# Kernel tuning notes

Measured on AMD Instinct MI355X. Metric: run time of the kernel, lower is better.

## Reference

```python
import jax, jax.numpy as jnp
import numpy as np

TAU, RHO, OFFSET, DELTA, START = 0.01, 100.0, 1.44, 0.05, 0.5
N_LEVELS = 3


def _heaviside(x):
    # torch.heaviside(x, values=1.0): 0 for x<0, 1 for x==0, 1 for x>0
    return jnp.where(x < 0, 0.0, 1.0).astype(x.dtype)


def _tau_sigmoid(x, tau):
    # 1 / (1 + exp(clamp(-x/tau, -50, 50)))
    e = jnp.clip(-x / tau, -50.0, 50.0)
    return 1.0 / (1.0 + jnp.exp(e))


def _step_rank(x, target):
    # x: [B, B, B] score diffs; target: [B, B] int relevance counts
    # inferior_relevance[b, i, j] = target[b, i] > target[b, j]
    inferior = target[:, :, None] > target[:, None, :]
    pos = x > 0
    margin = x > DELTA
    sig = _tau_sigmoid(x, TAU)
    pos_branch = jnp.where(margin, RHO * (x - DELTA) + OFFSET, START + sig)
    inf_val = jnp.where(pos, pos_branch, sig)
    return jnp.where(inferior, inf_val, _heaviside(x))


def setup_inputs() -> dict:
    key = jax.random.key(0)
    k1, k2 = jax.random.split(key)
    B, D = 384, 512
    emb = jax.random.normal(k1, (B, D), dtype=jnp.float32)
    emb = emb / jnp.linalg.norm(emb, axis=-1, keepdims=True)  # cosine-sim embeddings
    labels = jax.random.randint(k2, (B, N_LEVELS), 0, 8, dtype=jnp.int64)
    return {"embeddings": emb, "labels": labels}


def reference(embeddings, labels):
    B = embeddings.shape[0]
    scores = embeddings @ embeddings.T                      # [B, B]
    # create_label_matrix: count of matching hierarchy levels
    target = (labels[:, None, :] == labels[None, :, :]).sum(-1)  # [B, B] int
    relevances = target.astype(scores.dtype) / N_LEVELS          # [B, B]

    mask = 1.0 - jnp.eye(B, dtype=scores.dtype)             # [B, B] (broadcast over batch)
    # sim_diff[b, i, j] = scores[b, j] - scores[b, i]
    sim_diff = scores[:, None, :] - scores[:, :, None]      # [B, B, B]
    min_rel = jnp.minimum(relevances[:, :, None], relevances[:, None, :])

    rank = 1.0 + jnp.sum(_step_rank(sim_diff, target) * mask, axis=-1)      # [B, B]
    hrank = relevances + jnp.sum(_heaviside(sim_diff) * min_rel * mask, axis=-1)

    mhap = (hrank / rank).sum(-1) / relevances.sum(-1)      # [B]
    return jnp.mean(1.0 - mhap)                             # return_type='1-mHAP', reduce='mean'
```

## Files before the change

kernel.cpp:

```cpp
#include <hip/hip_runtime.h>
#include <hip/hip_bf16.h>

#define NB 384
#define ND 512

__global__ __launch_bounds__(256) void gemm_scores(const float* __restrict__ emb,
                                                   float* __restrict__ s0,
                                                   float* __restrict__ s1) {
    __shared__ float As[32][65];
    __shared__ float Bs[32][65];
    const int tid = threadIdx.x;
    const int tx = tid & 15, ty = tid >> 4;
    const int i0 = blockIdx.y * 32, j0 = blockIdx.x * 32;
    const int kbase = blockIdx.z * (ND / 2);
    float* __restrict__ s = blockIdx.z ? s1 : s0;
    float acc00 = 0.f, acc01 = 0.f, acc10 = 0.f, acc11 = 0.f;

    for (int k0 = kbase; k0 < kbase + ND / 2; k0 += 64) {
#pragma unroll
        for (int p = 0; p < 2; ++p) {
            int idx = tid + 256 * p;
            int r = idx >> 4;
            int c = (idx & 15) << 2;
            float4 av = *reinterpret_cast<const float4*>(emb + (i0 + r) * ND + k0 + c);
            As[r][c] = av.x; As[r][c + 1] = av.y; As[r][c + 2] = av.z; As[r][c + 3] = av.w;
            float4 bv = *reinterpret_cast<const float4*>(emb + (j0 + r) * ND + k0 + c);
            Bs[r][c] = bv.x; Bs[r][c + 1] = bv.y; Bs[r][c + 2] = bv.z; Bs[r][c + 3] = bv.w;
        }
        __syncthreads();
#pragma unroll 8
        for (int kk = 0; kk < 64; ++kk) {
            float a0 = As[2 * ty][kk], a1 = As[2 * ty + 1][kk];
            float b0 = Bs[2 * tx][kk], b1 = Bs[2 * tx + 1][kk];
            acc00 = fmaf(a0, b0, acc00); acc01 = fmaf(a0, b1, acc01);
            acc10 = fmaf(a1, b0, acc10); acc11 = fmaf(a1, b1, acc11);
        }
        __syncthreads();
    }
    const int i = i0 + 2 * ty, j = j0 + 2 * tx;
    s[i * NB + j]           = acc00; s[i * NB + j + 1]       = acc01;
    s[(i + 1) * NB + j]     = acc10; s[(i + 1) * NB + j + 1] = acc11;
}

__global__ __launch_bounds__(NB) void hap_prep(const float* __restrict__ s0,
                                               const float* __restrict__ s1,
                                               const int* __restrict__ labels,
                                               float* __restrict__ g,
                                               int* __restrict__ offs,
                                               float* __restrict__ tsumArr) {
    __shared__ int wcnt[6][4];
    __shared__ int wbase[6][4];
    __shared__ int cbase[4];
    const int tid = threadIdx.x, lane = tid & 63, wv = tid >> 6;
    const int b = blockIdx.x;
    const int l0 = labels[b * 3 + 0], l1 = labels[b * 3 + 1], l2 = labels[b * 3 + 2];
    const int t = (labels[tid * 3 + 0] == l0) + (labels[tid * 3 + 1] == l1) +
                  (labels[tid * 3 + 2] == l2);
    const float sv = s0[b * NB + tid] + s1[b * NB + tid];
    const unsigned long long mlt = (1ull << lane) - 1ull;
    int myrank = 0;
#pragma unroll
    for (int c = 0; c < 4; ++c) {
        unsigned long long m = __ballot(t == c);
        if (t == c) myrank = __popcll(m & mlt);
        if (lane == 0) wcnt[wv][c] = __popcll(m);
    }
    __syncthreads();
    if (tid == 0) {
        int tot0 = 0, tot1 = 0, tot2 = 0, tot3 = 0;
        for (int w = 0; w < 6; ++w) {
            wbase[w][0] = tot0; tot0 += wcnt[w][0];
            wbase[w][1] = tot1; tot1 += wcnt[w][1];
            wbase[w][2] = tot2; tot2 += wcnt[w][2];
            wbase[w][3] = tot3; tot3 += wcnt[w][3];
        }
        cbase[0] = 0; cbase[1] = tot0; cbase[2] = tot0 + tot1; cbase[3] = tot0 + tot1 + tot2;
        offs[b * 4 + 0] = cbase[1];
        offs[b * 4 + 1] = cbase[2];
        offs[b * 4 + 2] = cbase[3];
        tsumArr[b] = (float)(tot1 + 2 * tot2 + 3 * tot3);
    }
    __syncthreads();
    g[b * NB + cbase[t] + wbase[wv][t] + myrank] = sv;
}

__global__ __launch_bounds__(192) void hap_part(const float* __restrict__ g,
                                                const int* __restrict__ offs,
                                                float2* __restrict__ part) {
    __shared__ alignas(16) float gs[96];
    const int tid = threadIdx.x;
    const int b = blockIdx.x, ih = blockIdx.y, jh = blockIdx.z;
    const int q0 = jh * 96;

    if (tid < 96) gs[tid] = g[b * NB + q0 + tid];
    const int i = ih * 192 + tid;
    const float si = g[b * NB + i];
    const int S1 = offs[b * 4 + 0], S2 = offs[b * 4 + 1], S3 = offs[b * 4 + 2];
    const int ti = (i >= S1) + (i >= S2) + (i >= S3);
    __syncthreads();

    const int Rti = (ti == 0) ? 0 : (ti == 1) ? S1 : (ti == 2) ? S2 : S3;
    int m = Rti - q0; m = m < 0 ? 0 : (m > 96 ? 96 : m);

    const float nsiK = si * 144.26950408889634f;
    const float pconst = fmaf(-100.f, si, -3.56f);
    const float c1 = si + 0.05f;

    float rs = 0.f, hs = 0.f;
    int k = 0;
#pragma unroll 4
    for (; k < m; ++k) {
        const float sj = gs[k];
        const float ex = __builtin_amdgcn_exp2f(fmaf(sj, -144.26950408889634f, nsiK));
        const float sg = __builtin_amdgcn_rcpf(1.f + ex);
        const float posb = fmaf(100.f, sj, pconst);
        const float sel = (sj > c1) ? posb : (0.5f + sg);
        rs += (sj > si) ? sel : sg;
        const int pos = q0 + k;
        const float wk = (float)((pos >= S1) + (pos >= S2));
        hs += (sj >= si) ? wk : 0.f;
    }
    int cnt = 0;
#pragma unroll 8
    for (; k < 96; ++k) cnt += (gs[k] >= si) ? 1 : 0;

    rs += (float)cnt;
    hs += (float)(ti * cnt);
    part[(jh * NB + b) * NB + i] = make_float2(rs, hs);
}

__global__ __launch_bounds__(192) void hap_combine(const float2* __restrict__ part,
                                                   const float* __restrict__ tsumArr,
                                                   float* __restrict__ bsum) {
    __shared__ float redQ[3];
    const int tid = threadIdx.x, lane = tid & 63, wv = tid >> 6;
    const int b = blockIdx.x;
    float q = 0.f;
#pragma unroll
    for (int rep = 0; rep < 2; ++rep) {
        const int i = rep * 192 + tid;
        float r = 0.f, h = 0.f;
#pragma unroll
        for (int jh = 0; jh < 4; ++jh) {
            const float2 p = part[(jh * NB + b) * NB + i];
            r += p.x; h += p.y;
        }
        q += h / r;
    }
#pragma unroll
    for (int off = 32; off > 0; off >>= 1) q += __shfl_xor(q, off, 64);
    if (lane == 0) redQ[wv] = q;
    __syncthreads();
    if (tid == 0) bsum[b] = (redQ[0] + redQ[1] + redQ[2]) / (tsumArr[b] * (float)NB);
}

__global__ __launch_bounds__(64) void hap_final(const float* __restrict__ bsum,
                                                float* __restrict__ out) {
    const int tid = threadIdx.x;
    float p = 0.f;
    for (int k = tid; k < NB; k += 64) p += bsum[k];
#pragma unroll
    for (int off = 32; off > 0; off >>= 1) p += __shfl_xor(p, off, 64);
    if (tid == 0) out[0] = 1.f - p;
}

extern "C" void kernel_launch(void* const* d_in, const int* in_sizes, int n_in,
                              void* d_out, int out_size, void* d_ws, size_t ws_size,
                              hipStream_t stream) {
    const float* emb = (const float*)d_in[0];
    const int* labels = (const int*)d_in[1];
    float* out = (float*)d_out;

    float* s0 = (float*)d_ws;
    float* s1 = s0 + NB * NB;
    float* g  = s1 + NB * NB;
    float2* part = (float2*)(g + NB * NB);
    int* offs = (int*)(part + 4 * NB * NB);
    float* tsumArr = (float*)(offs + NB * 4);
    float* bsum = tsumArr + NB;

    gemm_scores<<<dim3(12, 12, 2), 256, 0, stream>>>(emb, s0, s1);
    hap_prep<<<NB, NB, 0, stream>>>(s0, s1, labels, g, offs, tsumArr);
    hap_part<<<dim3(NB, 2, 4), 192, 0, stream>>>(g, offs, part);
    hap_combine<<<NB, 192, 0, stream>>>(part, tsumArr, bsum);
    hap_final<<<1, 64, 0, stream>>>(bsum, out);
}
```

Before: 46.06 us.

## Fuse prep, partial and combine kernels; retile GEMM with 8-way split-K

Merges the bucket-sort prep, pairwise partial, and combine kernels into one kernel per (row, quarter). Each block redoes the label-grouped sort in shared memory and reduces its partials with shuffles instead of writing intermediate arrays. The GEMM moves to 64x64 tiles with 4x4 register blocking, a transposed LDS layout with float4 reads, and 8 split-K slices. This cuts launches and global round trips, but the sort and the 8-slice score summation are now repeated 4 times per row.

```diff
diff --git a/kernel.cpp b/kernel.cpp
--- a/kernel.cpp
+++ b/kernel.cpp
@@ -3,66 +3,83 @@
 
 #define NB 384
 #define ND 512
+#define NZ 8
 
 __global__ __launch_bounds__(256) void gemm_scores(const float* __restrict__ emb,
-                                                   float* __restrict__ s0,
-                                                   float* __restrict__ s1) {
-    __shared__ float As[32][65];
-    __shared__ float Bs[32][65];
+                                                   float* __restrict__ sp) {
+    __shared__ alignas(16) float At[64 * 68];
+    __shared__ alignas(16) float Bt[64 * 68];
     const int tid = threadIdx.x;
+    const int i0 = blockIdx.y * 64, j0 = blockIdx.x * 64;
+    const int kb = blockIdx.z * 64;
+    float* __restrict__ s = sp + blockIdx.z * (NB * NB);
+
+#pragma unroll
+    for (int p = 0; p < 4; ++p) {
+        const int idx = tid + 256 * p;
+        const int r = idx >> 4;
+        const int c4 = (idx & 15) << 2;
+        const float4 av = *reinterpret_cast<const float4*>(emb + (i0 + r) * ND + kb + c4);
+        At[(c4 + 0) * 68 + r] = av.x;
+        At[(c4 + 1) * 68 + r] = av.y;
+        At[(c4 + 2) * 68 + r] = av.z;
+        At[(c4 + 3) * 68 + r] = av.w;
+        const float4 bv = *reinterpret_cast<const float4*>(emb + (j0 + r) * ND + kb + c4);
+        Bt[(c4 + 0) * 68 + r] = bv.x;
+        Bt[(c4 + 1) * 68 + r] = bv.y;
+        Bt[(c4 + 2) * 68 + r] = bv.z;
+        Bt[(c4 + 3) * 68 + r] = bv.w;
+    }
+    __syncthreads();
+
     const int tx = tid & 15, ty = tid >> 4;
-    const int i0 = blockIdx.y * 32, j0 = blockIdx.x * 32;
-    const int kbase = blockIdx.z * (ND / 2);
-    float* __restrict__ s = blockIdx.z ? s1 : s0;
-    float acc00 = 0.f, acc01 = 0.f, acc10 = 0.f, acc11 = 0.f;
-
-    for (int k0 = kbase; k0 < kbase + ND / 2; k0 += 64) {
+    float acc[4][4] = {};
+#pragma unroll 4
+    for (int kk = 0; kk < 64; ++kk) {
+        const float4 a = *reinterpret_cast<const float4*>(&At[kk * 68 + ty * 4]);
+        const float4 b = *reinterpret_cast<const float4*>(&Bt[kk * 68 + tx * 4]);
+        acc[0][0] = fmaf(a.x, b.x, acc[0][0]); acc[0][1] = fmaf(a.x, b.y, acc[0][1]);
+        acc[0][2] = fmaf(a.x, b.z, acc[0][2]); acc[0][3] = fmaf(a.x, b.w, acc[0][3]);
+        acc[1][0] = fmaf(a.y, b.x, acc[1][0]); acc[1][1] = fmaf(a.y, b.y, acc[1][1]);
+        acc[1][2] = fmaf(a.y, b.z, acc[1][2]); acc[1][3] = fmaf(a.y, b.w, acc[1][3]);
+        acc[2][0] = fmaf(a.z, b.x, acc[2][0]); acc[2][1] = fmaf(a.z, b.y, acc[2][1]);
+        acc[2][2] = fmaf(a.z, b.z, acc[2][2]); acc[2][3] = fmaf(a.z, b.w, acc[2][3]);
+        acc[3][0] = fmaf(a.w, b.x, acc[3][0]); acc[3][1] = fmaf(a.w, b.y, acc[3][1]);
+        acc[3][2] = fmaf(a.w, b.z, acc[3][2]); acc[3][3] = fmaf(a.w, b.w, acc[3][3]);
+    }
 #pragma unroll
-        for (int p = 0; p < 2; ++p) {
-            int idx = tid + 256 * p;
-            int r = idx >> 4;
-            int c = (idx & 15) << 2;
-            float4 av = *reinterpret_cast<const float4*>(emb + (i0 + r) * ND + k0 + c);
-            As[r][c] = av.x; As[r][c + 1] = av.y; As[r][c + 2] = av.z; As[r][c + 3] = av.w;
-            float4 bv = *reinterpret_cast<const float4*>(emb + (j0 + r) * ND + k0 + c);
-            Bs[r][c] = bv.x; Bs[r][c + 1] = bv.y; Bs[r][c + 2] = bv.z; Bs[r][c + 3] = bv.w;
-        }
-        __syncthreads();
-#pragma unroll 8
-        for (int kk = 0; kk < 64; ++kk) {
-            float a0 = As[2 * ty][kk], a1 = As[2 * ty + 1][kk];
-            float b0 = Bs[2 * tx][kk], b1 = Bs[2 * tx + 1][kk];
-            acc00 = fmaf(a0, b0, acc00); acc01 = fmaf(a0, b1, acc01);
-            acc10 = fmaf(a1, b0, acc10); acc11 = fmaf(a1, b1, acc11);
-        }
-        __syncthreads();
+    for (int u = 0; u < 4; ++u) {
+        float4 o = make_float4(acc[u][0], acc[u][1], acc[u][2], acc[u][3]);
+        *reinterpret_cast<float4*>(&s[(i0 + ty * 4 + u) * NB + j0 + tx * 4]) = o;
     }
-    const int i = i0 + 2 * ty, j = j0 + 2 * tx;
-    s[i * NB + j]           = acc00; s[i * NB + j + 1]       = acc01;
-    s[(i + 1) * NB + j]     = acc10; s[(i + 1) * NB + j + 1] = acc11;
 }
 
-__global__ __launch_bounds__(NB) void hap_prep(const float* __restrict__ s0,
-                                               const float* __restrict__ s1,
-                                               const int* __restrict__ labels,
-                                               float* __restrict__ g,
-                                               int* __restrict__ offs,
-                                               float* __restrict__ tsumArr) {
+__global__ __launch_bounds__(384) void hap_fused(const float* __restrict__ sp,
+                                                 const int* __restrict__ labels,
+                                                 float* __restrict__ bpart) {
+    __shared__ alignas(16) float gs[NB];
     __shared__ int wcnt[6][4];
     __shared__ int wbase[6][4];
-    __shared__ int cbase[4];
+    __shared__ int cb[4];
+    __shared__ float tsum_sh;
+    __shared__ float redQ[6];
+
     const int tid = threadIdx.x, lane = tid & 63, wv = tid >> 6;
-    const int b = blockIdx.x;
+    const int b = blockIdx.x, iq = blockIdx.y;
+
     const int l0 = labels[b * 3 + 0], l1 = labels[b * 3 + 1], l2 = labels[b * 3 + 2];
     const int t = (labels[tid * 3 + 0] == l0) + (labels[tid * 3 + 1] == l1) +
                   (labels[tid * 3 + 2] == l2);
-    const float sv = s0[b * NB + tid] + s1[b * NB + tid];
+    float sv = 0.f;
+#pragma unroll
+    for (int z = 0; z < NZ; ++z) sv += sp[z * NB * NB + b * NB + tid];
+
     const unsigned long long mlt = (1ull << lane) - 1ull;
-    int myrank = 0;
+    int rk = 0;
 #pragma unroll
     for (int c = 0; c < 4; ++c) {
         unsigned long long m = __ballot(t == c);
-        if (t == c) myrank = __popcll(m & mlt);
+        if (t == c) rk = __popcll(m & mlt);
         if (lane == 0) wcnt[wv][c] = __popcll(m);
     }
     __syncthreads();
@@ -74,94 +91,72 @@
             wbase[w][2] = tot2; tot2 += wcnt[w][2];
             wbase[w][3] = tot3; tot3 += wcnt[w][3];
         }
-        cbase[0] = 0; cbase[1] = tot0; cbase[2] = tot0 + tot1; cbase[3] = tot0 + tot1 + tot2;
-        offs[b * 4 + 0] = cbase[1];
-        offs[b * 4 + 1] = cbase[2];
-        offs[b * 4 + 2] = cbase[3];
-        tsumArr[b] = (float)(tot1 + 2 * tot2 + 3 * tot3);
+        cb[0] = 0; cb[1] = tot0; cb[2] = tot0 + tot1; cb[3] = tot0 + tot1 + tot2;
+        tsum_sh = (float)(tot1 + 2 * tot2 + 3 * tot3);
     }
     __syncthreads();
-    g[b * NB + cbase[t] + wbase[wv][t] + myrank] = sv;
-}
-
-__global__ __launch_bounds__(192) void hap_part(const float* __restrict__ g,
-                                                const int* __restrict__ offs,
-                                                float2* __restrict__ part) {
-    __shared__ alignas(16) float gs[96];
-    const int tid = threadIdx.x;
-    const int b = blockIdx.x, ih = blockIdx.y, jh = blockIdx.z;
-    const int q0 = jh * 96;
-
-    if (tid < 96) gs[tid] = g[b * NB + q0 + tid];
-    const int i = ih * 192 + tid;
-    const float si = g[b * NB + i];
-    const int S1 = offs[b * 4 + 0], S2 = offs[b * 4 + 1], S3 = offs[b * 4 + 2];
-    const int ti = (i >= S1) + (i >= S2) + (i >= S3);
+    gs[cb[t] + wbase[wv][t] + rk] = sv;
     __syncthreads();
 
+    const int S1 = cb[1], S2 = cb[2], S3 = cb[3];
+    const int it = tid >> 2, jt = tid & 3;
+    const int i = iq * 96 + it;
+    const float si = gs[i];
+    const int ti = (i >= S1) + (i >= S2) + (i >= S3);
     const int Rti = (ti == 0) ? 0 : (ti == 1) ? S1 : (ti == 2) ? S2 : S3;
-    int m = Rti - q0; m = m < 0 ? 0 : (m > 96 ? 96 : m);
 
-    const float nsiK = si * 144.26950408889634f;
+    const float siK = si * 144.26950408889634f;
     const float pconst = fmaf(-100.f, si, -3.56f);
     const float c1 = si + 0.05f;
 
-    float rs = 0.f, hs = 0.f;
-    int k = 0;
-#pragma unroll 4
-    for (; k < m; ++k) {
+    float rs = 0.f;
+    int hsI = 0, cnt = 0;
+    for (int k = jt; k < Rti; k += 4) {
         const float sj = gs[k];
-        const float ex = __builtin_amdgcn_exp2f(fmaf(sj, -144.26950408889634f, nsiK));
+        const float ex = __builtin_amdgcn_exp2f(fmaf(sj, -144.26950408889634f, siK));
         const float sg = __builtin_amdgcn_rcpf(1.f + ex);
-        const float posb = fmaf(100.f, sj, pconst);
-        const float sel = (sj > c1) ? posb : (0.5f + sg);
+        const float ramp = fmaf(100.f, sj, pconst);
+        const float sel = (sj > c1) ? ramp : (0.5f + sg);
         rs += (sj > si) ? sel : sg;
-        const int pos = q0 + k;
-        const float wk = (float)((pos >= S1) + (pos >= S2));
-        hs += (sj >= si) ? wk : 0.f;
+        const int wk = (k >= S1) + (k >= S2);
+        hsI += (sj >= si) ? wk : 0;
     }
-    int cnt = 0;
-#pragma unroll 8
-    for (; k < 96; ++k) cnt += (gs[k] >= si) ? 1 : 0;
+    const int a0 = (Rti + 3) & ~3;
+    if (Rti + jt < a0) cnt += (gs[Rti + jt] >= si) ? 1 : 0;
+    const float4* gv = reinterpret_cast<const float4*>(gs);
+    for (int k4 = (a0 >> 2) + jt; k4 < (NB >> 2); k4 += 4) {
+        const float4 v = gv[k4];
+        cnt += ((v.x >= si) ? 1 : 0) + ((v.y >= si) ? 1 : 0) +
+               ((v.z >= si) ? 1 : 0) + ((v.w >= si) ? 1 : 0);
+    }
+    rs += (float)cnt;
+    hsI += ti * cnt;
 
-    rs += (float)cnt;
-    hs += (float)(ti * cnt);
-    part[(jh * NB + b) * NB + i] = make_float2(rs, hs);
-}
-
-__global__ __launch_bounds__(192) void hap_combine(const float2* __restrict__ part,
-                                                   const float* __restrict__ tsumArr,
-                                                   float* __restrict__ bsum) {
-    __shared__ float redQ[3];
-    const int tid = threadIdx.x, lane = tid & 63, wv = tid >> 6;
-    const int b = blockIdx.x;
-    float q = 0.f;
-#pragma unroll
-    for (int rep = 0; rep < 2; ++rep) {
-        const int i = rep * 192 + tid;
-        float r = 0.f, h = 0.f;
-#pragma unroll
-        for (int jh = 0; jh < 4; ++jh) {
-            const float2 p = part[(jh * NB + b) * NB + i];
-            r += p.x; h += p.y;
-        }
-        q += h / r;
-    }
+    rs += __shfl_xor(rs, 1); rs += __shfl_xor(rs, 2);
+    float hs = (float)hsI;
+    hs += __shfl_xor(hs, 1); hs += __shfl_xor(hs, 2);
+    float q = hs / rs;
 #pragma unroll
     for (int off = 32; off > 0; off >>= 1) q += __shfl_xor(q, off, 64);
     if (lane == 0) redQ[wv] = q;
     __syncthreads();
-    if (tid == 0) bsum[b] = (redQ[0] + redQ[1] + redQ[2]) / (tsumArr[b] * (float)NB);
+    if (tid == 0) {
+        const float tot = redQ[0] + redQ[1] + redQ[2] + redQ[3] + redQ[4] + redQ[5];
+        bpart[b * 4 + iq] = tot / (4.f * tsum_sh * (float)NB);
+    }
 }
 
-__global__ __launch_bounds__(64) void hap_final(const float* __restrict__ bsum,
-                                                float* __restrict__ out) {
-    const int tid = threadIdx.x;
+__global__ __launch_bounds__(256) void hap_final(const float* __restrict__ bpart,
+                                                 float* __restrict__ out) {
+    __shared__ float red[4];
+    const int tid = threadIdx.x, lane = tid & 63, wv = tid >> 6;
     float p = 0.f;
-    for (int k = tid; k < NB; k += 64) p += bsum[k];
+    for (int k = tid; k < NB * 4; k += 256) p += bpart[k];
 #pragma unroll
     for (int off = 32; off > 0; off >>= 1) p += __shfl_xor(p, off, 64);
-    if (tid == 0) out[0] = 1.f - p;
+    if (lane == 0) red[wv] = p;
+    __syncthreads();
+    if (tid == 0) out[0] = 1.f - (red[0] + red[1] + red[2] + red[3]);
 }
 
 extern "C" void kernel_launch(void* const* d_in, const int* in_sizes, int n_in,
@@ -171,17 +166,10 @@
     const int* labels = (const int*)d_in[1];
     float* out = (float*)d_out;
 
-    float* s0 = (float*)d_ws;
-    float* s1 = s0 + NB * NB;
-    float* g  = s1 + NB * NB;
-    float2* part = (float2*)(g + NB * NB);
-    int* offs = (int*)(part + 4 * NB * NB);
-    float* tsumArr = (float*)(offs + NB * 4);
-    float* bsum = tsumArr + NB;
+    float* sp = (float*)d_ws;
+    float* bpart = sp + NZ * NB * NB;
 
-    gemm_scores<<<dim3(12, 12, 2), 256, 0, stream>>>(emb, s0, s1);
-    hap_prep<<<NB, NB, 0, stream>>>(s0, s1, labels, g, offs, tsumArr);
-    hap_part<<<dim3(NB, 2, 4), 192, 0, stream>>>(g, offs, part);
-    hap_combine<<<NB, 192, 0, stream>>>(part, tsumArr, bsum);
-    hap_final<<<1, 64, 0, stream>>>(bsum, out);
+    gemm_scores<<<dim3(6, 6, NZ), 256, 0, stream>>>(emb, sp);
+    hap_fused<<<dim3(NB, 4), 384, 0, stream>>>(sp, labels, bpart);
+    hap_final<<<1, 256, 0, stream>>>(bpart, out);
 }
```

Result: faster. 38.73 us (-15.9%).
